# Kernel tuning notes

Measured on AMD Instinct MI355X. Metric: run time of the kernel, lower is better.

The kernel has to match this reference:

```python
import jax, jax.numpy as jnp
from jax import lax
import numpy as np

QMAX = 127.0  # int8 symmetric quant range


def setup_inputs() -> dict:
    key = jax.random.key(0)
    k1, k2, k3, k4 = jax.random.split(key, 4)
    B, S, D_in, D_out = 4, 2048, 4096, 4096
    x = jax.random.normal(k1, (B, S, D_in), dtype=jnp.float32)
    # pre-quantized per-channel weights [output_size, input_size]
    weight_q = jax.random.randint(k2, (D_out, D_in), -127, 128, dtype=jnp.int32).astype(jnp.int8)
    weight_scale = (jax.random.uniform(k3, (D_out,), dtype=jnp.float32) + 0.5) * 0.01
    bias = jax.random.normal(k4, (D_out,), dtype=jnp.float32) * 0.02
    return {"x": x, "weight_q": weight_q, "weight_scale": weight_scale, "bias": bias}


def reference(x, weight_q, weight_scale, bias):
    """Dynamic per-token int8 activation quant + int8 matmul + dequant + bias.

    x: [..., D_in] float32; weight_q: [D_out, D_in] int8;
    weight_scale: [D_out]; bias: [D_out]. Returns [..., D_out] float32.
    """
    orig_shape = x.shape
    x2 = x.reshape(-1, orig_shape[-1])  # [T, D_in]
    # dynamic per-token symmetric quantization
    amax = jnp.max(jnp.abs(x2), axis=-1, keepdims=True)  # [T, 1]
    x_scale = jnp.maximum(amax, 1e-8) / QMAX
    x_q = jnp.clip(jnp.round(x2 / x_scale), -128.0, QMAX).astype(jnp.int8)
    acc = lax.dot_general(x_q, weight_q, (((1,), (1,)), ((), ())),
                          preferred_element_type=jnp.int32)  # [T, D_out]
    out = acc.astype(jnp.float32) * x_scale * weight_scale[None, :]
    out = out.reshape(*orig_shape[:-1], out.shape[-1]) + bias
    return out
```

## Files before the change

### kernel.cpp

```cpp
#include <hip/hip_runtime.h>

typedef __attribute__((ext_vector_type(4))) int int4v;

#define BM 128
#define BN 128
#define BK 64

__global__ __launch_bounds__(256) void pack_w_kernel(const int* __restrict__ w32,
                                                     int* __restrict__ w8,
                                                     long n4) {
    long i = (long)blockIdx.x * 256 + threadIdx.x;
    if (i >= n4) return;
    int4v v = ((const int4v*)w32)[i];
    w8[i] = (v[0] & 0xFF) | ((v[1] & 0xFF) << 8) |
            ((v[2] & 0xFF) << 16) | ((v[3] & 0xFF) << 24);
}

template <int NCHUNK>
__global__ __launch_bounds__(256) void quant_kernel(const float* __restrict__ x,
                                                    signed char* __restrict__ xq,
                                                    float* __restrict__ xs,
                                                    int K) {
    const int t = blockIdx.x;
    const int tid = threadIdx.x;
    const float4* row = (const float4*)(x + (size_t)t * K);

    float4 v[NCHUNK];
    float amax = 0.0f;
    #pragma unroll
    for (int i = 0; i < NCHUNK; ++i) {
        float4 f = row[i * 256 + tid];
        v[i] = f;
        amax = fmaxf(amax, fmaxf(fmaxf(fabsf(f.x), fabsf(f.y)),
                                 fmaxf(fabsf(f.z), fabsf(f.w))));
    }
    #pragma unroll
    for (int off = 32; off >= 1; off >>= 1)
        amax = fmaxf(amax, __shfl_xor(amax, off, 64));
    __shared__ float red[4];
    if ((tid & 63) == 0) red[tid >> 6] = amax;
    __syncthreads();
    amax = fmaxf(fmaxf(red[0], red[1]), fmaxf(red[2], red[3]));

    const float scale = fmaxf(amax, 1e-8f) / 127.0f;
    if (tid == 0) xs[t] = scale;
    const float inv = 1.0f / scale;

    int* orow = (int*)(xq + (size_t)t * K);
    #pragma unroll
    for (int i = 0; i < NCHUNK; ++i) {
        float4 f = v[i];
        int q0 = (int)fminf(fmaxf(rintf(f.x * inv), -128.0f), 127.0f);
        int q1 = (int)fminf(fmaxf(rintf(f.y * inv), -128.0f), 127.0f);
        int q2 = (int)fminf(fmaxf(rintf(f.z * inv), -128.0f), 127.0f);
        int q3 = (int)fminf(fmaxf(rintf(f.w * inv), -128.0f), 127.0f);
        orow[i * 256 + tid] =
            (q0 & 0xFF) | ((q1 & 0xFF) << 8) | ((q2 & 0xFF) << 16) | ((q3 & 0xFF) << 24);
    }
}

__global__ __launch_bounds__(256) void gemm_i8_kernel(
    const signed char* __restrict__ A,
    const signed char* __restrict__ B,
    const float* __restrict__ xs,
    const float* __restrict__ wsc,
    const float* __restrict__ bias,
    float* __restrict__ C,
    int M, int N, int K) {
    __shared__ __align__(16) signed char sA[BM * BK];
    __shared__ __align__(16) signed char sB[BN * BK];

    const int tid = threadIdx.x;
    const int lane = tid & 63;
    const int wave = tid >> 6;
    const int bm = blockIdx.y * BM;
    const int bn = blockIdx.x * BN;
    const int wm = (wave >> 1) * 64;
    const int wn = (wave & 1) * 64;

    const signed char* ag = A + (size_t)(bm + wave * 32 + (lane >> 2)) * K + (lane & 3) * 16;
    const signed char* bg = B + (size_t)(bn + wave * 32 + (lane >> 2)) * K + (lane & 3) * 16;
    signed char* la = sA + (wave * 32) * BK;
    signed char* lb = sB + (wave * 32) * BK;

    const int mrow = lane & 15;
    const int ksub = (lane >> 4) * 16;
    const signed char* ra = sA + (size_t)(wm + mrow) * BK + ksub;
    const signed char* rb = sB + (size_t)(wn + mrow) * BK + ksub;

    int4v acc[4][4];
    const int4v zero = {0, 0, 0, 0};
    #pragma unroll
    for (int i = 0; i < 4; ++i)
        #pragma unroll
        for (int j = 0; j < 4; ++j)
            acc[i][j] = zero;

    for (int k0 = 0; k0 < K; k0 += BK) {
        #pragma unroll
        for (int j = 0; j < 2; ++j) {
            __builtin_amdgcn_global_load_lds(
                (const __attribute__((address_space(1))) void*)(ag + (size_t)j * 16 * K),
                (__attribute__((address_space(3))) void*)(la + j * 16 * BK), 16, 0, 0);
            __builtin_amdgcn_global_load_lds(
                (const __attribute__((address_space(1))) void*)(bg + (size_t)j * 16 * K),
                (__attribute__((address_space(3))) void*)(lb + j * 16 * BK), 16, 0, 0);
        }
        ag += BK;
        bg += BK;
        __syncthreads();

        int4v af[4], bf[4];
        #pragma unroll
        for (int i = 0; i < 4; ++i) {
            af[i] = *(const int4v*)(ra + i * 16 * BK);
            bf[i] = *(const int4v*)(rb + i * 16 * BK);
        }
        #pragma unroll
        for (int i = 0; i < 4; ++i)
            #pragma unroll
            for (int j = 0; j < 4; ++j)
                acc[i][j] = __builtin_amdgcn_mfma_i32_16x16x64_i8(af[i], bf[j], acc[i][j], 0, 0, 0);

        __syncthreads();
    }

    const int nl = lane & 15;
    const int quad = lane >> 4;
    float wv[4], bv[4];
    #pragma unroll
    for (int j = 0; j < 4; ++j) {
        wv[j] = wsc[bn + wn + j * 16 + nl];
        bv[j] = bias[bn + wn + j * 16 + nl];
    }
    #pragma unroll
    for (int i = 0; i < 4; ++i) {
        #pragma unroll
        for (int r = 0; r < 4; ++r) {
            const int row = bm + wm + i * 16 + quad * 4 + r;
            const float s = xs[row];
            float* crow = C + (size_t)row * N + bn + wn + nl;
            #pragma unroll
            for (int j = 0; j < 4; ++j)
                crow[j * 16] = (float)acc[i][j][r] * s * wv[j] + bv[j];
        }
    }
}

extern "C" void kernel_launch(void* const* d_in, const int* in_sizes, int n_in,
                              void* d_out, int out_size, void* d_ws, size_t ws_size,
                              hipStream_t stream) {
    const float* x = (const float*)d_in[0];
    const int* wq32 = (const int*)d_in[1];
    const float* wscale = (const float*)d_in[2];
    const float* bias = (const float*)d_in[3];
    float* out = (float*)d_out;

    const int d_out_dim = in_sizes[2];
    const int d_in_dim = in_sizes[1] / d_out_dim;
    const int T = in_sizes[0] / d_in_dim;

    const size_t wbytes = (size_t)d_out_dim * d_in_dim;
    signed char* w8 = (signed char*)d_ws;
    signed char* xq = (signed char*)d_ws + wbytes;
    float* xscl = (float*)((char*)d_ws + wbytes + (size_t)T * d_in_dim);

    const long n4 = (long)d_out_dim * d_in_dim / 4;
    pack_w_kernel<<<(int)((n4 + 255) / 256), 256, 0, stream>>>(wq32, (int*)w8, n4);

    if (d_in_dim == 4096) {
        quant_kernel<4><<<T, 256, 0, stream>>>(x, xq, xscl, d_in_dim);
    } else {
        quant_kernel<8><<<T, 256, 0, stream>>>(x, xq, xscl, d_in_dim);
    }

    dim3 grid(d_out_dim / BN, T / BM);
    gemm_i8_kernel<<<grid, 256, 0, stream>>>(xq, w8, xscl, wscale, bias, out,
                                             T, d_out_dim, d_in_dim);
}
```

Measured before the change: 439.8 us.

## Rewrite int8 GEMM with 256x256 tiles, 8 waves, double-buffered swizzled LDS pipeline

Replaces the simple 128x128 tile GEMM, which loads then syncs every step, with a 256x256 tile, 512-thread kernel. It double-buffers A and B tiles in LDS, issues the global-to-LDS loads for later K tiles while MFMAs run on the current ones, and XOR-swizzles the LDS layout to avoid bank conflicts. It also uses s_setprio and explicit waitcnt/barrier scheduling to interleave loads with compute. The aim is to hide memory latency and raise arithmetic intensity, at the cost of much higher register and LDS usage and fragile hand-written synchronisation.

```diff
diff --git a/kernel.cpp b/kernel.cpp
--- a/kernel.cpp
+++ b/kernel.cpp
@@ -1,10 +1,6 @@
 #include <hip/hip_runtime.h>
 
 typedef __attribute__((ext_vector_type(4))) int int4v;
-
-#define BM 128
-#define BN 128
-#define BK 64
 
 __global__ __launch_bounds__(256) void pack_w_kernel(const int* __restrict__ w32,
                                                      int* __restrict__ w8,
@@ -59,7 +55,71 @@
     }
 }
 
-__global__ __launch_bounds__(256) void gemm_i8_kernel(
+#define BM 256
+#define BN 256
+#define BKB 128
+
+#define MFMA_I8 __builtin_amdgcn_mfma_i32_16x16x64_i8
+
+#define BARRIER()                       \
+    do {                                \
+        __builtin_amdgcn_s_barrier();   \
+        asm volatile("" ::: "memory");  \
+    } while (0)
+
+#define LGKM0() asm volatile("s_waitcnt lgkmcnt(0)" ::: "memory")
+#define VMCNT4() asm volatile("s_waitcnt vmcnt(4)" ::: "memory")
+
+#define STAGE_HALF(GL, LB, ROWOFF, KK)                                        \
+    do {                                                                      \
+        __builtin_amdgcn_global_load_lds(                                     \
+            (const __attribute__((address_space(1))) void*)(                  \
+                (GL) + (size_t)(ROWOFF) * K + (KK)),                          \
+            (__attribute__((address_space(3))) void*)((LB) + (ROWOFF) * BKB), \
+            16, 0, 0);                                                        \
+        __builtin_amdgcn_global_load_lds(                                     \
+            (const __attribute__((address_space(1))) void*)(                  \
+                (GL) + (size_t)((ROWOFF) + 64) * K + (KK)),                   \
+            (__attribute__((address_space(3))) void*)(                        \
+                (LB) + ((ROWOFF) + 64) * BKB),                                \
+            16, 0, 0);                                                        \
+    } while (0)
+
+#define LDA4(RP, MOFF)                                                     \
+    do {                                                                   \
+        af[0][0] = *(const int4v*)((RP) + ((MOFF) + 0) * 2048 + sw0);      \
+        af[0][1] = *(const int4v*)((RP) + ((MOFF) + 0) * 2048 + sw1);      \
+        af[1][0] = *(const int4v*)((RP) + ((MOFF) + 1) * 2048 + sw0);      \
+        af[1][1] = *(const int4v*)((RP) + ((MOFF) + 1) * 2048 + sw1);      \
+        af[2][0] = *(const int4v*)((RP) + ((MOFF) + 2) * 2048 + sw0);      \
+        af[2][1] = *(const int4v*)((RP) + ((MOFF) + 2) * 2048 + sw1);      \
+        af[3][0] = *(const int4v*)((RP) + ((MOFF) + 3) * 2048 + sw0);      \
+        af[3][1] = *(const int4v*)((RP) + ((MOFF) + 3) * 2048 + sw1);      \
+    } while (0)
+
+#define LDB2M(RP, NB)                                                      \
+    do {                                                                   \
+        bf[(NB) + 0][0] = *(const int4v*)((RP) + ((NB) + 0) * 2048 + sw0); \
+        bf[(NB) + 0][1] = *(const int4v*)((RP) + ((NB) + 0) * 2048 + sw1); \
+        bf[(NB) + 1][0] = *(const int4v*)((RP) + ((NB) + 1) * 2048 + sw0); \
+        bf[(NB) + 1][1] = *(const int4v*)((RP) + ((NB) + 1) * 2048 + sw1); \
+    } while (0)
+
+#define QUAD(MB, NB)                                                          \
+    do {                                                                      \
+        _Pragma("unroll") for (int m_ = 0; m_ < 4; ++m_) {                    \
+            _Pragma("unroll") for (int n_ = 0; n_ < 2; ++n_) {                \
+                acc[(MB) + m_][(NB) + n_] = MFMA_I8(                          \
+                    af[m_][0], bf[(NB) + n_][0], acc[(MB) + m_][(NB) + n_],   \
+                    0, 0, 0);                                                 \
+                acc[(MB) + m_][(NB) + n_] = MFMA_I8(                          \
+                    af[m_][1], bf[(NB) + n_][1], acc[(MB) + m_][(NB) + n_],   \
+                    0, 0, 0);                                                 \
+            }                                                                 \
+        }                                                                     \
+    } while (0)
+
+__global__ __launch_bounds__(512, 2) void gemm_i8_kernel(
     const signed char* __restrict__ A,
     const signed char* __restrict__ B,
     const float* __restrict__ xs,
@@ -67,82 +127,155 @@
     const float* __restrict__ bias,
     float* __restrict__ C,
     int M, int N, int K) {
-    __shared__ __align__(16) signed char sA[BM * BK];
-    __shared__ __align__(16) signed char sB[BN * BK];
+    __shared__ __align__(16) signed char lds[2][2][BM * BKB];
 
     const int tid = threadIdx.x;
     const int lane = tid & 63;
-    const int wave = tid >> 6;
+    const int wv = tid >> 6;
+    const int wrow = wv >> 2;
+    const int wcol = wv & 3;
+    const int fr = lane & 15;
+    const int q = lane >> 4;
+
     const int bm = blockIdx.y * BM;
     const int bn = blockIdx.x * BN;
-    const int wm = (wave >> 1) * 64;
-    const int wn = (wave & 1) * 64;
-
-    const signed char* ag = A + (size_t)(bm + wave * 32 + (lane >> 2)) * K + (lane & 3) * 16;
-    const signed char* bg = B + (size_t)(bn + wave * 32 + (lane >> 2)) * K + (lane & 3) * 16;
-    signed char* la = sA + (wave * 32) * BK;
-    signed char* lb = sB + (wave * 32) * BK;
-
-    const int mrow = lane & 15;
-    const int ksub = (lane >> 4) * 16;
-    const signed char* ra = sA + (size_t)(wm + mrow) * BK + ksub;
-    const signed char* rb = sB + (size_t)(wn + mrow) * BK + ksub;
-
-    int4v acc[4][4];
+
+    const int srow = wv * 8 + (lane >> 3);
+    const int scol = ((lane & 7) ^ ((lane >> 3) & 7)) << 4;
+    const signed char* gA = A + (size_t)(bm + srow) * K + scol;
+    const signed char* gB = B + (size_t)(bn + srow) * K + scol;
+
+    signed char* wA0 = &lds[0][0][0] + wv * 1024;
+    signed char* wA1 = &lds[1][0][0] + wv * 1024;
+    signed char* wB0 = &lds[0][1][0] + wv * 1024;
+    signed char* wB1 = &lds[1][1][0] + wv * 1024;
+
+    const int rowA = (wrow * 128 + fr) * BKB;
+    const int rowB = (wcol * 64 + fr) * BKB;
+    const int sw0 = ((0 + q) ^ (fr & 7)) << 4;
+    const int sw1 = ((4 + q) ^ (fr & 7)) << 4;
+    const signed char* rA0 = &lds[0][0][0] + rowA;
+    const signed char* rA1 = &lds[1][0][0] + rowA;
+    const signed char* rB0 = &lds[0][1][0] + rowB;
+    const signed char* rB1 = &lds[1][1][0] + rowB;
+
+    int4v acc[8][4];
     const int4v zero = {0, 0, 0, 0};
     #pragma unroll
-    for (int i = 0; i < 4; ++i)
+    for (int m = 0; m < 8; ++m)
         #pragma unroll
-        for (int j = 0; j < 4; ++j)
-            acc[i][j] = zero;
-
-    for (int k0 = 0; k0 < K; k0 += BK) {
-        #pragma unroll
-        for (int j = 0; j < 2; ++j) {
-            __builtin_amdgcn_global_load_lds(
-                (const __attribute__((address_space(1))) void*)(ag + (size_t)j * 16 * K),
-                (__attribute__((address_space(3))) void*)(la + j * 16 * BK), 16, 0, 0);
-            __builtin_amdgcn_global_load_lds(
-                (const __attribute__((address_space(1))) void*)(bg + (size_t)j * 16 * K),
-                (__attribute__((address_space(3))) void*)(lb + j * 16 * BK), 16, 0, 0);
-        }
-        ag += BK;
-        bg += BK;
-        __syncthreads();
-
-        int4v af[4], bf[4];
-        #pragma unroll
-        for (int i = 0; i < 4; ++i) {
-            af[i] = *(const int4v*)(ra + i * 16 * BK);
-            bf[i] = *(const int4v*)(rb + i * 16 * BK);
-        }
-        #pragma unroll
-        for (int i = 0; i < 4; ++i)
-            #pragma unroll
-            for (int j = 0; j < 4; ++j)
-                acc[i][j] = __builtin_amdgcn_mfma_i32_16x16x64_i8(af[i], bf[j], acc[i][j], 0, 0, 0);
-
-        __syncthreads();
-    }
-
-    const int nl = lane & 15;
-    const int quad = lane >> 4;
-    float wv[4], bv[4];
-    #pragma unroll
-    for (int j = 0; j < 4; ++j) {
-        wv[j] = wsc[bn + wn + j * 16 + nl];
-        bv[j] = bias[bn + wn + j * 16 + nl];
-    }
-    #pragma unroll
-    for (int i = 0; i < 4; ++i) {
+        for (int n = 0; n < 4; ++n) acc[m][n] = zero;
+    int4v af[4][2], bf[4][2];
+
+    STAGE_HALF(gA, wA0, 0, 0);
+    STAGE_HALF(gA, wA0, 128, 0);
+    STAGE_HALF(gB, wB0, 0, 0);
+    STAGE_HALF(gB, wB0, 128, 0);
+    STAGE_HALF(gB, wB1, 0, (size_t)BKB);
+    STAGE_HALF(gB, wB1, 128, (size_t)BKB);
+    VMCNT4();
+    BARRIER();
+
+    const int NT = K / BKB;
+    for (int i = 0; i < NT / 2; ++i) {
+        const size_t kk1 = (size_t)(2 * i + 1) * BKB;
+        int t2 = 2 * i + 2; if (t2 >= NT) t2 -= NT;
+        int t3 = 2 * i + 3; if (t3 >= NT) t3 -= NT;
+        const size_t kk2 = (size_t)t2 * BKB;
+        const size_t kk3 = (size_t)t3 * BKB;
+
+        LDA4(rA0, 0);
+        LDB2M(rB0, 0);
+        STAGE_HALF(gA, wA1, 0, kk1);
+        BARRIER();
+        LGKM0();
+        __builtin_amdgcn_s_setprio(1);
+        QUAD(0, 0);
+        __builtin_amdgcn_s_setprio(0);
+        BARRIER();
+
+        LDB2M(rB0, 2);
+        STAGE_HALF(gA, wA1, 128, kk1);
+        BARRIER();
+        LGKM0();
+        __builtin_amdgcn_s_setprio(1);
+        QUAD(0, 2);
+        __builtin_amdgcn_s_setprio(0);
+        BARRIER();
+
+        LDA4(rA0, 4);
+        STAGE_HALF(gB, wB0, 0, kk2);
+        BARRIER();
+        LGKM0();
+        __builtin_amdgcn_s_setprio(1);
+        QUAD(4, 2);
+        __builtin_amdgcn_s_setprio(0);
+        BARRIER();
+
+        STAGE_HALF(gB, wB0, 128, kk2);
+        VMCNT4();
+        BARRIER();
+        __builtin_amdgcn_s_setprio(1);
+        QUAD(4, 0);
+        __builtin_amdgcn_s_setprio(0);
+        BARRIER();
+
+        LDA4(rA1, 0);
+        LDB2M(rB1, 0);
+        STAGE_HALF(gA, wA0, 0, kk2);
+        BARRIER();
+        LGKM0();
+        __builtin_amdgcn_s_setprio(1);
+        QUAD(0, 0);
+        __builtin_amdgcn_s_setprio(0);
+        BARRIER();
+
+        LDB2M(rB1, 2);
+        STAGE_HALF(gA, wA0, 128, kk2);
+        BARRIER();
+        LGKM0();
+        __builtin_amdgcn_s_setprio(1);
+        QUAD(0, 2);
+        __builtin_amdgcn_s_setprio(0);
+        BARRIER();
+
+        LDA4(rA1, 4);
+        STAGE_HALF(gB, wB1, 0, kk3);
+        BARRIER();
+        LGKM0();
+        __builtin_amdgcn_s_setprio(1);
+        QUAD(4, 2);
+        __builtin_amdgcn_s_setprio(0);
+        BARRIER();
+
+        STAGE_HALF(gB, wB1, 128, kk3);
+        VMCNT4();
+        BARRIER();
+        __builtin_amdgcn_s_setprio(1);
+        QUAD(4, 0);
+        __builtin_amdgcn_s_setprio(0);
+        BARRIER();
+    }
+
+    asm volatile("s_waitcnt vmcnt(0)" ::: "memory");
+
+    const int cb = bn + wcol * 64;
+    float wv4[4], bv4[4];
+    #pragma unroll
+    for (int n = 0; n < 4; ++n) {
+        wv4[n] = wsc[cb + n * 16 + fr];
+        bv4[n] = bias[cb + n * 16 + fr];
+    }
+    #pragma unroll
+    for (int m = 0; m < 8; ++m) {
         #pragma unroll
         for (int r = 0; r < 4; ++r) {
-            const int row = bm + wm + i * 16 + quad * 4 + r;
+            const int row = bm + wrow * 128 + m * 16 + q * 4 + r;
             const float s = xs[row];
-            float* crow = C + (size_t)row * N + bn + wn + nl;
+            float* crow = C + (size_t)row * N + cb + fr;
             #pragma unroll
-            for (int j = 0; j < 4; ++j)
-                crow[j * 16] = (float)acc[i][j][r] * s * wv[j] + bv[j];
+            for (int n = 0; n < 4; ++n)
+                crow[n * 16] = (float)acc[m][n][r] * s * wv4[n] + bv4[n];
         }
     }
 }
@@ -175,6 +308,6 @@
     }
 
     dim3 grid(d_out_dim / BN, T / BM);
-    gemm_i8_kernel<<<grid, 256, 0, stream>>>(xq, w8, xscl, wscale, bias, out,
+    gemm_i8_kernel<<<grid, 512, 0, stream>>>(xq, w8, xscl, wscale, bias, out,
                                              T, d_out_dim, d_in_dim);
 }
```

After: 383.0 us. 1.15x faster.
